# Performance work log

Hardware: AMD Instinct MI355X
Metric: run time of the kernel (lower is better)

The kernel has to match this reference:

```python
import jax, jax.numpy as jnp
import numpy as np

# --- dimensions (must match init_kwargs / input_specs) ---
N = 512      # memory_size
WORD = 64    # word_size
R = 4        # num_reads
NW = 1       # num_writes
C = 512      # controller_output_size
B = 16       # batch
T = 32       # seq_len
MODES = 3    # num_read_modes
IF = R*WORD + R + NW*WORD + NW + NW*WORD + NW*WORD + R + NW + NW + R*MODES  # 471
EPS = 1e-8


def _parse_interface(v):
    # v: [B, IF] -> dict of gates/keys, mirroring _parse_interface_vector
    i = 0
    def take(n):
        nonlocal i
        s = v[:, i:i+n]
        i += n
        return s
    read_keys = take(R*WORD).reshape(-1, R, WORD)
    read_strengths = jax.nn.softplus(take(R))
    write_keys = take(NW*WORD).reshape(-1, NW, WORD)
    write_strengths = jax.nn.softplus(take(NW))
    erase_vectors = jax.nn.sigmoid(take(NW*WORD)).reshape(-1, NW, WORD)
    write_vectors = take(NW*WORD).reshape(-1, NW, WORD)
    free_gates = jax.nn.sigmoid(take(R))
    allocation_gates = jax.nn.sigmoid(take(NW))
    write_gates = jax.nn.sigmoid(take(NW))
    read_modes = jax.nn.softmax(take(R*MODES).reshape(-1, R, MODES), axis=-1)
    return dict(read_keys=read_keys, read_strengths=read_strengths,
                write_keys=write_keys, write_strengths=write_strengths,
                erase_vectors=erase_vectors, write_vectors=write_vectors,
                free_gates=free_gates, allocation_gates=allocation_gates,
                write_gates=write_gates, read_modes=read_modes)


def _content_weights(keys, strengths, memory):
    # cosine content addressing: keys [B,H,WORD], memory [B,N,WORD] -> [B,H,N]
    kn = keys * jax.lax.rsqrt(jnp.sum(keys*keys, -1, keepdims=True) + EPS)
    mn = memory * jax.lax.rsqrt(jnp.sum(memory*memory, -1, keepdims=True) + EPS)
    sim = jnp.einsum('bhw,bnw->bhn', kn, mn)
    return jax.nn.softmax(sim * strengths[..., None], axis=-1)


def _allocation(usage):
    # usage [B,N] -> allocation weighting [B,N] (DNC usage-sorted free-list)
    idx = jnp.argsort(usage, axis=-1)                      # ascending usage
    sorted_u = jnp.take_along_axis(usage, idx, axis=-1)
    cp = jnp.cumprod(sorted_u, axis=-1)
    excl = jnp.concatenate([jnp.ones_like(cp[:, :1]), cp[:, :-1]], axis=-1)
    a_sorted = (1.0 - sorted_u) * excl
    inv = jnp.argsort(idx, axis=-1)                        # unsort
    return jnp.take_along_axis(a_sorted, inv, axis=-1)


def _forward(controller_output, W_if, b_if):
    eye = jnp.eye(N, dtype=controller_output.dtype)

    def step(carry, ctrl_t):
        memory, rw, ww, link, prec, usage = carry
        p = _parse_interface(ctrl_t @ W_if + b_if)
        # write weights: content + allocation, gated
        wcw = _content_weights(p['write_keys'], p['write_strengths'], memory)  # [B,NW,N]
        alloc = _allocation(usage)[:, None, :]
        ag = p['allocation_gates'][..., None]
        wg = p['write_gates'][..., None]
        new_ww = wg * (ag * alloc + (1.0 - ag) * wcw)                           # [B,NW,N]
        # usage update (write bump then free-gate retention)
        ww_agg = 1.0 - jnp.prod(1.0 - new_ww, axis=1)                           # [B,N]
        u = usage + ww_agg - usage * ww_agg
        psi = jnp.prod(1.0 - p['free_gates'][..., None] * rw, axis=1)           # [B,N]
        new_usage = u * psi
        # memory erase + write
        erase_term = jnp.prod(1.0 - new_ww[:, :, :, None] * p['erase_vectors'][:, :, None, :], axis=1)
        new_mem = memory * erase_term + jnp.einsum('bhn,bhw->bnw', new_ww, p['write_vectors'])
        # temporal linkage (write heads summed as in the source)
        wsum = jnp.sum(new_ww, axis=1)                                          # [B,N]
        new_link = (1.0 - wsum[:, :, None] - wsum[:, None, :]) * link \
                   + wsum[:, :, None] * prec[:, None, :]
        new_link = new_link * (1.0 - eye)
        new_prec = (1.0 - jnp.sum(wsum, axis=-1, keepdims=True)) * prec + wsum
        # read weights: backward / content / forward modes
        rcw = _content_weights(p['read_keys'], p['read_strengths'], new_mem)    # [B,R,N]
        fwd = jnp.einsum('bij,brj->bri', new_link, rw)
        bwd = jnp.einsum('bji,brj->bri', new_link, rw)
        m = p['read_modes']
        new_rw = m[..., 0:1] * bwd + m[..., 1:2] * rcw + m[..., 2:3] * fwd      # [B,R,N]
        read_words = jnp.einsum('brn,bnw->brw', new_rw, new_mem)                # [B,R,WORD]
        return (new_mem, new_rw, new_ww, new_link, new_prec, new_usage), read_words

    dt = controller_output.dtype
    init = (jnp.zeros((B, N, WORD), dt),
            jnp.full((B, R, N), 1.0 / N, dt),
            jnp.full((B, NW, N), 1.0 / N, dt),
            jnp.zeros((B, N, N), dt),
            jnp.zeros((B, N), dt),
            jnp.zeros((B, N), dt))
    _, rws = jax.lax.scan(step, init, jnp.swapaxes(controller_output, 0, 1))
    return jnp.swapaxes(rws, 0, 1)  # [B,T,R,WORD]


def setup_inputs() -> dict:
    key = jax.random.key(0)
    k1, k2 = jax.random.split(key)
    controller_output = jax.random.normal(k1, (B, T, C), dtype=jnp.float32)
    W_if = jax.random.normal(k2, (C, IF), dtype=jnp.float32) * 0.05  # keep gates unsaturated
    b_if = jnp.zeros((IF,), dtype=jnp.float32)
    return {"controller_output": controller_output, "W_if": W_if, "b_if": b_if}


def reference(controller_output, W_if, b_if):
    return _forward(controller_output, W_if, b_if)
```

## Files before the change

kernel.cpp:

```cpp
#include <hip/hip_runtime.h>

#define NCELLS 512
#define WORD_SZ 64
#define RHEADS 4
#define BATCH 16
#define TSTEPS 32
#define IFSZ 471
#define EPSC 1e-8f
#define NSTRIPE 16

__device__ __forceinline__ float wave_sum(float v) {
#pragma unroll
  for (int m = 32; m >= 1; m >>= 1) v += __shfl_xor(v, m, 64);
  return v;
}
__device__ __forceinline__ float wave_max(float v) {
#pragma unroll
  for (int m = 32; m >= 1; m >>= 1) v = fmaxf(v, __shfl_xor(v, m, 64));
  return v;
}
__device__ __forceinline__ float block_sum(float v, float* s_red, int tid) {
  float w = wave_sum(v);
  if ((tid & 63) == 0) s_red[tid >> 6] = w;
  __syncthreads();
  float tot = 0.f;
#pragma unroll
  for (int i = 0; i < 8; i++) tot += s_red[i];
  __syncthreads();
  return tot;
}
__device__ __forceinline__ float block_max(float v, float* s_red, int tid) {
  float w = wave_max(v);
  if ((tid & 63) == 0) s_red[tid >> 6] = w;
  __syncthreads();
  float tot = s_red[0];
#pragma unroll
  for (int i = 1; i < 8; i++) tot = fmaxf(tot, s_red[i]);
  __syncthreads();
  return tot;
}
__device__ __forceinline__ float softplus_f(float x) {
  return fmaxf(x, 0.f) + log1pf(expf(-fabsf(x)));
}
__device__ __forceinline__ float sigmoid_f(float x) {
  return 1.f / (1.f + expf(-x));
}

__global__ void init_kernel(float* link, float* mem, float* rw, float* usage,
                            float* prec, float* wcwb, float* ppb) {
  size_t i = (size_t)blockIdx.x * blockDim.x + threadIdx.x;
  size_t stride = (size_t)gridDim.x * blockDim.x;
  const size_t nlink = (size_t)BATCH * NCELLS * NCELLS;
  const size_t nmem = (size_t)BATCH * NCELLS * WORD_SZ;
  const size_t nrw = (size_t)BATCH * RHEADS * NCELLS;
  const size_t nu = (size_t)BATCH * NCELLS;
  for (size_t x = i; x < nlink; x += stride) link[x] = 0.f;
  for (size_t x = i; x < nmem; x += stride) mem[x] = 0.f;
  for (size_t x = i; x < nrw; x += stride) rw[x] = 1.f / NCELLS;
  for (size_t x = i; x < nu; x += stride) {
    usage[x] = 0.f; prec[x] = 0.f;
    wcwb[x] = 1.f / NCELLS;
    ppb[0 * nu + x] = ((x & (NCELLS - 1)) == 0) ? 1.f : 0.f;
    ppb[1 * nu + x] = 1.f;
    ppb[2 * nu + x] = 1.f;
    ppb[3 * nu + x] = 1.f;
  }
}

__global__ __launch_bounds__(512) void iface_kernel(
    const float* __restrict__ ctrl, const float* __restrict__ W,
    const float* __restrict__ bif, float* __restrict__ iface) {
  int bt = blockIdx.x;
  int tid = threadIdx.x;
  __shared__ float s_ctrl[512];
  __shared__ float s_v[IFSZ];
  s_ctrl[tid] = ctrl[(size_t)bt * 512 + tid];
  __syncthreads();
  if (tid < IFSZ) {
    float acc = bif[tid];
#pragma unroll 8
    for (int k = 0; k < 512; k++) acc = fmaf(s_ctrl[k], W[(size_t)k * IFSZ + tid], acc);
    s_v[tid] = acc;
  }
  __syncthreads();
  if (tid < IFSZ) {
    float v = s_v[tid];
    float o;
    if (tid < 256) o = v;
    else if (tid < 260) o = softplus_f(v);
    else if (tid < 324) o = v;
    else if (tid < 325) o = softplus_f(v);
    else if (tid < 389) o = sigmoid_f(v);
    else if (tid < 453) o = v;
    else if (tid < 459) o = sigmoid_f(v);
    else {
      int g = (tid - 459) / 3;
      int base = 459 + g * 3;
      float a = s_v[base], b = s_v[base + 1], c = s_v[base + 2];
      float mx = fmaxf(a, fmaxf(b, c));
      float ea = expf(a - mx), eb = expf(b - mx), ec = expf(c - mx);
      o = expf(v - mx) / (ea + eb + ec);
    }
    iface[(size_t)bt * IFSZ + tid] = o;
  }
}

__global__ __launch_bounds__(512) void step_link(
    const float* __restrict__ iface,
    const float* __restrict__ mem_old, float* __restrict__ mem_new,
    const float* __restrict__ usage_old, float* __restrict__ usage_new,
    const float* __restrict__ prec_old, float* __restrict__ prec_new,
    const float* __restrict__ rw_old,
    const float* __restrict__ wcwb, const float* __restrict__ ppb,
    float* __restrict__ link, float* __restrict__ fwd, float* __restrict__ bwdp,
    int t) {
  int stripe = blockIdx.x, b = blockIdx.y;
  int tid = threadIdx.x, lane = tid & 63, wid = tid >> 6;
  int n = tid;
  const float* ifc = iface + ((size_t)b * TSTEPS + t) * IFSZ;

  __shared__ float s_e[64], s_v[64];
  __shared__ float s_ww[512], s_prec[512], s_rw4[4][512];
  __shared__ float s_bpB[4][4][512];
  __shared__ float s_red[8];

  if (wid == 0 && stripe == 0) { s_e[lane] = ifc[325 + lane]; s_v[lane] = ifc[389 + lane]; }

  size_t bn = (size_t)b * NCELLS;
  const size_t BN = (size_t)BATCH * NCELLS;
  float u_n = usage_old[bn + n];
  float wcw = wcwb[bn + n];
  float p01 = ppb[0 * BN + bn + n] * ppb[1 * BN + bn + n];
  float p23 = ppb[2 * BN + bn + n] * ppb[3 * BN + bn + n];
  float allocv = (1.f - u_n) * (p01 * p23);
  float ag = ifc[457], wg = ifc[458];
  float wwn = wg * (ag * allocv + (1.f - ag) * wcw);
  s_ww[n] = wwn;
  s_prec[n] = prec_old[bn + n];
#pragma unroll
  for (int r = 0; r < 4; r++) s_rw4[r][n] = rw_old[(bn * RHEADS) + (size_t)r * NCELLS + n];
  __syncthreads();

  float* lbase = link + (size_t)b * NCELLS * NCELLS;
  int i0 = stripe * 32 + wid * 4;
  float wsi[4], rwi[4][4];
#pragma unroll
  for (int rr = 0; rr < 4; rr++) {
    wsi[rr] = s_ww[i0 + rr];
#pragma unroll
    for (int r = 0; r < 4; r++) rwi[rr][r] = s_rw4[r][i0 + rr];
  }
  float facc[4][4];
  float bc[4][8];
#pragma unroll
  for (int a = 0; a < 4; a++)
#pragma unroll
    for (int c = 0; c < 4; c++) facc[a][c] = 0.f;
#pragma unroll
  for (int a = 0; a < 4; a++)
#pragma unroll
    for (int c = 0; c < 8; c++) bc[a][c] = 0.f;

#pragma unroll
  for (int jj = 0; jj < 8; jj++) {
    int j = jj * 64 + lane;
    float swj = s_ww[j], spj = s_prec[j];
    float srw0 = s_rw4[0][j], srw1 = s_rw4[1][j], srw2 = s_rw4[2][j], srw3 = s_rw4[3][j];
#pragma unroll
    for (int rr = 0; rr < 4; rr++) {
      float* lp = lbase + (size_t)(i0 + rr) * NCELLS + j;
      float l = *lp;
      float ln = fmaf(1.f - wsi[rr] - swj, l, wsi[rr] * spj);
      if (j == i0 + rr) ln = 0.f;
      *lp = ln;
      facc[rr][0] = fmaf(ln, srw0, facc[rr][0]);
      facc[rr][1] = fmaf(ln, srw1, facc[rr][1]);
      facc[rr][2] = fmaf(ln, srw2, facc[rr][2]);
      facc[rr][3] = fmaf(ln, srw3, facc[rr][3]);
      bc[0][jj] = fmaf(ln, rwi[rr][0], bc[0][jj]);
      bc[1][jj] = fmaf(ln, rwi[rr][1], bc[1][jj]);
      bc[2][jj] = fmaf(ln, rwi[rr][2], bc[2][jj]);
      bc[3][jj] = fmaf(ln, rwi[rr][3], bc[3][jj]);
    }
  }
#pragma unroll
  for (int rr = 0; rr < 4; rr++) {
#pragma unroll
    for (int r = 0; r < 4; r++) facc[rr][r] = wave_sum(facc[rr][r]);
    if (lane == 0) {
#pragma unroll
      for (int r = 0; r < 4; r++)
        fwd[((size_t)b * RHEADS + r) * NCELLS + (i0 + rr)] = facc[rr][r];
    }
  }
  if (wid >= 4) {
#pragma unroll
    for (int r = 0; r < 4; r++)
#pragma unroll
      for (int jj = 0; jj < 8; jj++) s_bpB[wid - 4][r][jj * 64 + lane] = bc[r][jj];
  }
  __syncthreads();
  if (wid < 4) {
#pragma unroll
    for (int r = 0; r < 4; r++)
#pragma unroll
      for (int jj = 0; jj < 8; jj++) s_bpB[wid][r][jj * 64 + lane] += bc[r][jj];
  }
  __syncthreads();
#pragma unroll
  for (int r = 0; r < 4; r++) {
    float a = ((s_bpB[0][r][tid] + s_bpB[1][r][tid]) + (s_bpB[2][r][tid] + s_bpB[3][r][tid]));
    bwdp[(((size_t)stripe * BATCH + b) * RHEADS + r) * NCELLS + tid] = a;
  }

  if (stripe == 0) {
    const float* mo = mem_old + (size_t)b * NCELLS * WORD_SZ;
    float* mn = mem_new + (size_t)b * NCELLS * WORD_SZ;
#pragma unroll 4
    for (int kk = 0; kk < 64; kk++) {
      int flat = tid + kk * 512;
      int nn = flat >> 6, w = flat & 63;
      mn[flat] = fmaf(mo[flat], (1.f - s_ww[nn] * s_e[w]), s_ww[nn] * s_v[w]);
    }
  }
  if (stripe == 15) {
    float u = u_n + wwn - u_n * wwn;
    float psi = 1.f;
#pragma unroll
    for (int r = 0; r < 4; r++) psi *= (1.f - ifc[453 + r] * s_rw4[r][n]);
    usage_new[bn + n] = u * psi;
    float sw = block_sum(wwn, s_red, tid);
    prec_new[bn + n] = (1.f - sw) * s_prec[n] + wwn;
  }
}

__global__ __launch_bounds__(512) void read_step(
    const float* __restrict__ iface, const float* __restrict__ mem_new,
    const float* __restrict__ fwd, const float* __restrict__ bwdp,
    const float* __restrict__ usage_cur,
    float* __restrict__ rw_new, float* __restrict__ wcwb, float* __restrict__ ppb,
    float* __restrict__ out, int t) {
  int r = blockIdx.x, b = blockIdx.y;
  int tid = threadIdx.x, lane = tid & 63, wid = tid >> 6;
  int n = tid;
  const float* ifc = iface + ((size_t)b * TSTEPS + t) * IFSZ;
  bool have_next = (t + 1 < TSTEPS);
  const float* ifc2 = iface + ((size_t)b * TSTEPS + (have_next ? t + 1 : t)) * IFSZ;

  __shared__ float s_k[64], s_wk[64];
  __shared__ __align__(16) float s_u[512];
  __shared__ float s_rw[512];
  __shared__ float s_part[8][64];
  __shared__ float s_red[8];

  if (wid == 0) {
    float k = ifc[r * 64 + lane];
    float ss = wave_sum(k * k);
    s_k[lane] = k * rsqrtf(ss + EPSC);
  } else if (wid == 1 && have_next) {
    float k = ifc2[260 + lane];
    float ss = wave_sum(k * k);
    s_wk[lane] = k * rsqrtf(ss + EPSC);
  }
  if (have_next) s_u[tid] = usage_cur[(size_t)b * NCELLS + tid];
  __syncthreads();

  const float4* mrow = (const float4*)(mem_new + ((size_t)b * NCELLS + n) * WORD_SZ);
  bool do_w = (r == 0) && have_next;
  float msum = 0.f, dot = 0.f, dotw = 0.f;
#pragma unroll
  for (int i = 0; i < 16; i++) {
    float4 m4 = mrow[i];
    msum = fmaf(m4.x, m4.x, fmaf(m4.y, m4.y, fmaf(m4.z, m4.z, fmaf(m4.w, m4.w, msum))));
    dot = fmaf(m4.x, s_k[4 * i], fmaf(m4.y, s_k[4 * i + 1],
          fmaf(m4.z, s_k[4 * i + 2], fmaf(m4.w, s_k[4 * i + 3], dot))));
    if (do_w)
      dotw = fmaf(m4.x, s_wk[4 * i], fmaf(m4.y, s_wk[4 * i + 1],
             fmaf(m4.z, s_wk[4 * i + 2], fmaf(m4.w, s_wk[4 * i + 3], dotw))));
  }
  float minv = rsqrtf(msum + EPSC);
  float sim = dot * minv * ifc[256 + r];
  float mx = block_max(sim, s_red, tid);
  float e = expf(sim - mx);
  float ssum = block_sum(e, s_red, tid);
  float rcw = e / ssum;
  float bsum = 0.f;
#pragma unroll
  for (int s = 0; s < NSTRIPE; s++)
    bsum += bwdp[(((size_t)s * BATCH + b) * RHEADS + r) * NCELLS + n];
  float f = fwd[((size_t)b * RHEADS + r) * NCELLS + n];
  float m0 = ifc[459 + r * 3], m1 = ifc[459 + r * 3 + 1], m2 = ifc[459 + r * 3 + 2];
  float nrw = fmaf(m0, bsum, fmaf(m1, rcw, m2 * f));
  s_rw[n] = nrw;
  rw_new[((size_t)b * RHEADS + r) * NCELLS + n] = nrw;
  __syncthreads();

  float acc = 0.f;
  const float* mb = mem_new + (size_t)b * NCELLS * WORD_SZ;
#pragma unroll 8
  for (int k = 0; k < 64; k++) {
    int nn = wid * 64 + k;
    acc = fmaf(s_rw[nn], mb[(size_t)nn * WORD_SZ + lane], acc);
  }
  s_part[wid][lane] = acc;
  __syncthreads();
  if (tid < 64) {
    float a = 0.f;
#pragma unroll
    for (int w = 0; w < 8; w++) a += s_part[w][tid];
    out[(((size_t)b * TSTEPS + t) * RHEADS + r) * WORD_SZ + tid] = a;
  }

  if (have_next) {
    float un = s_u[n];
    int base = r * 128;
    float p0 = 1.f, p1 = 1.f, p2 = 1.f, p3 = 1.f;
#pragma unroll 8
    for (int j = 0; j < 128; j += 4) {
      float4 u4 = *(const float4*)&s_u[base + j];
      int ja = base + j;
      p0 *= (u4.x < un || (u4.x == un && (ja + 0) < n)) ? u4.x : 1.f;
      p1 *= (u4.y < un || (u4.y == un && (ja + 1) < n)) ? u4.y : 1.f;
      p2 *= (u4.z < un || (u4.z == un && (ja + 2) < n)) ? u4.z : 1.f;
      p3 *= (u4.w < un || (u4.w == un && (ja + 3) < n)) ? u4.w : 1.f;
    }
    ppb[((size_t)r * BATCH + b) * NCELLS + n] = (p0 * p1) * (p2 * p3);
    if (r == 0) {
      float simw = dotw * minv * ifc2[324];
      float mxw = block_max(simw, s_red, tid);
      float ew = expf(simw - mxw);
      float ssw = block_sum(ew, s_red, tid);
      wcwb[(size_t)b * NCELLS + n] = ew / ssw;
    }
  }
}

extern "C" void kernel_launch(void* const* d_in, const int* in_sizes, int n_in,
                              void* d_out, int out_size, void* d_ws, size_t ws_size,
                              hipStream_t stream) {
  const float* ctrl = (const float*)d_in[0];
  const float* Wif = (const float*)d_in[1];
  const float* bif = (const float*)d_in[2];
  float* out = (float*)d_out;

  float* p = (float*)d_ws;
  float* link = p;   p += (size_t)BATCH * NCELLS * NCELLS;
  float* mem0 = p;   p += (size_t)BATCH * NCELLS * WORD_SZ;
  float* mem1 = p;   p += (size_t)BATCH * NCELLS * WORD_SZ;
  float* iface = p;  p += (size_t)BATCH * TSTEPS * IFSZ;
  float* rw0 = p;    p += (size_t)BATCH * RHEADS * NCELLS;
  float* rw1 = p;    p += (size_t)BATCH * RHEADS * NCELLS;
  float* us0 = p;    p += (size_t)BATCH * NCELLS;
  float* us1 = p;    p += (size_t)BATCH * NCELLS;
  float* pr0 = p;    p += (size_t)BATCH * NCELLS;
  float* pr1 = p;    p += (size_t)BATCH * NCELLS;
  float* fwdb = p;   p += (size_t)BATCH * RHEADS * NCELLS;
  float* bwdp = p;   p += (size_t)NSTRIPE * BATCH * RHEADS * NCELLS;
  float* wcwb = p;   p += (size_t)BATCH * NCELLS;
  float* ppb = p;    p += (size_t)4 * BATCH * NCELLS;

  float* mem[2] = {mem0, mem1};
  float* rw[2] = {rw0, rw1};
  float* us[2] = {us0, us1};
  float* pr[2] = {pr0, pr1};

  hipLaunchKernelGGL(init_kernel, dim3(2048), dim3(256), 0, stream,
                     link, mem[0], rw[0], us[0], pr[0], wcwb, ppb);
  hipLaunchKernelGGL(iface_kernel, dim3(BATCH * TSTEPS), dim3(512), 0, stream,
                     ctrl, Wif, bif, iface);
  for (int t = 0; t < TSTEPS; t++) {
    int cu = t & 1;
    hipLaunchKernelGGL(step_link, dim3(NSTRIPE, BATCH), dim3(512), 0, stream,
                       iface, mem[cu], mem[cu ^ 1], us[cu], us[cu ^ 1],
                       pr[cu], pr[cu ^ 1], rw[cu], wcwb, ppb,
                       link, fwdb, bwdp, t);
    hipLaunchKernelGGL(read_step, dim3(RHEADS, BATCH), dim3(512), 0, stream,
                       iface, mem[cu ^ 1], fwdb, bwdp, us[cu ^ 1],
                       rw[cu ^ 1], wcwb, ppb, out, t);
  }
}
```

Before: 1.059 ms.

## Fuse timestep loop into persistent cooperative kernel with register-resident link matrix

Replaces the 64 per-timestep kernel launches with one cooperative persistent kernel of 256 blocks that loops over time and separates phases with grid-wide syncs. Each thread keeps its slice of the N×N link matrix in registers across all timesteps, so the 16 MB link matrix is no longer read and written in global memory each step, and its zero-initialisation is dropped. The memory update is now split across all stripes instead of one block. The costs are two grid syncs per step, high register pressure under launch_bounds(512,2), and a requirement that all 256 blocks be co-resident.

```diff
diff --git a/kernel.cpp b/kernel.cpp
--- a/kernel.cpp
+++ b/kernel.cpp
@@ -1,4 +1,7 @@
 #include <hip/hip_runtime.h>
+#include <hip/hip_cooperative_groups.h>
+
+namespace cg = cooperative_groups;
 
 #define NCELLS 512
 #define WORD_SZ 64
@@ -46,15 +49,13 @@
   return 1.f / (1.f + expf(-x));
 }
 
-__global__ void init_kernel(float* link, float* mem, float* rw, float* usage,
+__global__ void init_kernel(float* mem, float* rw, float* usage,
                             float* prec, float* wcwb, float* ppb) {
   size_t i = (size_t)blockIdx.x * blockDim.x + threadIdx.x;
   size_t stride = (size_t)gridDim.x * blockDim.x;
-  const size_t nlink = (size_t)BATCH * NCELLS * NCELLS;
   const size_t nmem = (size_t)BATCH * NCELLS * WORD_SZ;
   const size_t nrw = (size_t)BATCH * RHEADS * NCELLS;
   const size_t nu = (size_t)BATCH * NCELLS;
-  for (size_t x = i; x < nlink; x += stride) link[x] = 0.f;
   for (size_t x = i; x < nmem; x += stride) mem[x] = 0.f;
   for (size_t x = i; x < nrw; x += stride) rw[x] = 1.f / NCELLS;
   for (size_t x = i; x < nu; x += stride) {
@@ -105,233 +106,245 @@
   }
 }
 
-__global__ __launch_bounds__(512) void step_link(
+__global__ __launch_bounds__(512, 2) void dnc_loop(
     const float* __restrict__ iface,
-    const float* __restrict__ mem_old, float* __restrict__ mem_new,
-    const float* __restrict__ usage_old, float* __restrict__ usage_new,
-    const float* __restrict__ prec_old, float* __restrict__ prec_new,
-    const float* __restrict__ rw_old,
-    const float* __restrict__ wcwb, const float* __restrict__ ppb,
-    float* __restrict__ link, float* __restrict__ fwd, float* __restrict__ bwdp,
-    int t) {
-  int stripe = blockIdx.x, b = blockIdx.y;
-  int tid = threadIdx.x, lane = tid & 63, wid = tid >> 6;
-  int n = tid;
-  const float* ifc = iface + ((size_t)b * TSTEPS + t) * IFSZ;
-
+    float* __restrict__ mem0, float* __restrict__ mem1,
+    float* __restrict__ rw0, float* __restrict__ rw1,
+    float* __restrict__ us0, float* __restrict__ us1,
+    float* __restrict__ pr0, float* __restrict__ pr1,
+    float* __restrict__ wcwb, float* __restrict__ ppb,
+    float* __restrict__ fwdb, float* __restrict__ bwdp,
+    float* __restrict__ out) {
+  cg::grid_group grid = cg::this_grid();
+  const int blk = blockIdx.x;
+  const int stripe = blk >> 4, b = blk & 15;
+  const int tid = threadIdx.x, lane = tid & 63, wid = tid >> 6;
+  const int n = tid;
+  const size_t bn = (size_t)b * NCELLS;
+  const size_t BN = (size_t)BATCH * NCELLS;
+
+  __shared__ float s_ww[512], s_prec[512];
+  __shared__ float s_rw4[4][512];
+  __shared__ float s_bpB[4][4][512];
   __shared__ float s_e[64], s_v[64];
-  __shared__ float s_ww[512], s_prec[512], s_rw4[4][512];
-  __shared__ float s_bpB[4][4][512];
   __shared__ float s_red[8];
-
-  if (wid == 0 && stripe == 0) { s_e[lane] = ifc[325 + lane]; s_v[lane] = ifc[389 + lane]; }
-
-  size_t bn = (size_t)b * NCELLS;
-  const size_t BN = (size_t)BATCH * NCELLS;
-  float u_n = usage_old[bn + n];
-  float wcw = wcwb[bn + n];
-  float p01 = ppb[0 * BN + bn + n] * ppb[1 * BN + bn + n];
-  float p23 = ppb[2 * BN + bn + n] * ppb[3 * BN + bn + n];
-  float allocv = (1.f - u_n) * (p01 * p23);
-  float ag = ifc[457], wg = ifc[458];
-  float wwn = wg * (ag * allocv + (1.f - ag) * wcw);
-  s_ww[n] = wwn;
-  s_prec[n] = prec_old[bn + n];
-#pragma unroll
-  for (int r = 0; r < 4; r++) s_rw4[r][n] = rw_old[(bn * RHEADS) + (size_t)r * NCELLS + n];
-  __syncthreads();
-
-  float* lbase = link + (size_t)b * NCELLS * NCELLS;
-  int i0 = stripe * 32 + wid * 4;
-  float wsi[4], rwi[4][4];
-#pragma unroll
-  for (int rr = 0; rr < 4; rr++) {
-    wsi[rr] = s_ww[i0 + rr];
-#pragma unroll
-    for (int r = 0; r < 4; r++) rwi[rr][r] = s_rw4[r][i0 + rr];
-  }
-  float facc[4][4];
-  float bc[4][8];
-#pragma unroll
-  for (int a = 0; a < 4; a++)
-#pragma unroll
-    for (int c = 0; c < 4; c++) facc[a][c] = 0.f;
-#pragma unroll
-  for (int a = 0; a < 4; a++)
-#pragma unroll
-    for (int c = 0; c < 8; c++) bc[a][c] = 0.f;
-
-#pragma unroll
-  for (int jj = 0; jj < 8; jj++) {
-    int j = jj * 64 + lane;
-    float swj = s_ww[j], spj = s_prec[j];
-    float srw0 = s_rw4[0][j], srw1 = s_rw4[1][j], srw2 = s_rw4[2][j], srw3 = s_rw4[3][j];
-#pragma unroll
-    for (int rr = 0; rr < 4; rr++) {
-      float* lp = lbase + (size_t)(i0 + rr) * NCELLS + j;
-      float l = *lp;
-      float ln = fmaf(1.f - wsi[rr] - swj, l, wsi[rr] * spj);
-      if (j == i0 + rr) ln = 0.f;
-      *lp = ln;
-      facc[rr][0] = fmaf(ln, srw0, facc[rr][0]);
-      facc[rr][1] = fmaf(ln, srw1, facc[rr][1]);
-      facc[rr][2] = fmaf(ln, srw2, facc[rr][2]);
-      facc[rr][3] = fmaf(ln, srw3, facc[rr][3]);
-      bc[0][jj] = fmaf(ln, rwi[rr][0], bc[0][jj]);
-      bc[1][jj] = fmaf(ln, rwi[rr][1], bc[1][jj]);
-      bc[2][jj] = fmaf(ln, rwi[rr][2], bc[2][jj]);
-      bc[3][jj] = fmaf(ln, rwi[rr][3], bc[3][jj]);
-    }
-  }
-#pragma unroll
-  for (int rr = 0; rr < 4; rr++) {
-#pragma unroll
-    for (int r = 0; r < 4; r++) facc[rr][r] = wave_sum(facc[rr][r]);
-    if (lane == 0) {
-#pragma unroll
-      for (int r = 0; r < 4; r++)
-        fwd[((size_t)b * RHEADS + r) * NCELLS + (i0 + rr)] = facc[rr][r];
-    }
-  }
-  if (wid >= 4) {
-#pragma unroll
-    for (int r = 0; r < 4; r++)
-#pragma unroll
-      for (int jj = 0; jj < 8; jj++) s_bpB[wid - 4][r][jj * 64 + lane] = bc[r][jj];
-  }
-  __syncthreads();
-  if (wid < 4) {
-#pragma unroll
-    for (int r = 0; r < 4; r++)
-#pragma unroll
-      for (int jj = 0; jj < 8; jj++) s_bpB[wid][r][jj * 64 + lane] += bc[r][jj];
-  }
-  __syncthreads();
-#pragma unroll
-  for (int r = 0; r < 4; r++) {
-    float a = ((s_bpB[0][r][tid] + s_bpB[1][r][tid]) + (s_bpB[2][r][tid] + s_bpB[3][r][tid]));
-    bwdp[(((size_t)stripe * BATCH + b) * RHEADS + r) * NCELLS + tid] = a;
-  }
-
-  if (stripe == 0) {
-    const float* mo = mem_old + (size_t)b * NCELLS * WORD_SZ;
-    float* mn = mem_new + (size_t)b * NCELLS * WORD_SZ;
-#pragma unroll 4
-    for (int kk = 0; kk < 64; kk++) {
-      int flat = tid + kk * 512;
-      int nn = flat >> 6, w = flat & 63;
-      mn[flat] = fmaf(mo[flat], (1.f - s_ww[nn] * s_e[w]), s_ww[nn] * s_v[w]);
-    }
-  }
-  if (stripe == 15) {
-    float u = u_n + wwn - u_n * wwn;
-    float psi = 1.f;
-#pragma unroll
-    for (int r = 0; r < 4; r++) psi *= (1.f - ifc[453 + r] * s_rw4[r][n]);
-    usage_new[bn + n] = u * psi;
-    float sw = block_sum(wwn, s_red, tid);
-    prec_new[bn + n] = (1.f - sw) * s_prec[n] + wwn;
-  }
-}
-
-__global__ __launch_bounds__(512) void read_step(
-    const float* __restrict__ iface, const float* __restrict__ mem_new,
-    const float* __restrict__ fwd, const float* __restrict__ bwdp,
-    const float* __restrict__ usage_cur,
-    float* __restrict__ rw_new, float* __restrict__ wcwb, float* __restrict__ ppb,
-    float* __restrict__ out, int t) {
-  int r = blockIdx.x, b = blockIdx.y;
-  int tid = threadIdx.x, lane = tid & 63, wid = tid >> 6;
-  int n = tid;
-  const float* ifc = iface + ((size_t)b * TSTEPS + t) * IFSZ;
-  bool have_next = (t + 1 < TSTEPS);
-  const float* ifc2 = iface + ((size_t)b * TSTEPS + (have_next ? t + 1 : t)) * IFSZ;
-
   __shared__ float s_k[64], s_wk[64];
   __shared__ __align__(16) float s_u[512];
-  __shared__ float s_rw[512];
+  __shared__ float s_rwB[512];
   __shared__ float s_part[8][64];
-  __shared__ float s_red[8];
-
-  if (wid == 0) {
-    float k = ifc[r * 64 + lane];
-    float ss = wave_sum(k * k);
-    s_k[lane] = k * rsqrtf(ss + EPSC);
-  } else if (wid == 1 && have_next) {
-    float k = ifc2[260 + lane];
-    float ss = wave_sum(k * k);
-    s_wk[lane] = k * rsqrtf(ss + EPSC);
-  }
-  if (have_next) s_u[tid] = usage_cur[(size_t)b * NCELLS + tid];
-  __syncthreads();
-
-  const float4* mrow = (const float4*)(mem_new + ((size_t)b * NCELLS + n) * WORD_SZ);
-  bool do_w = (r == 0) && have_next;
-  float msum = 0.f, dot = 0.f, dotw = 0.f;
-#pragma unroll
-  for (int i = 0; i < 16; i++) {
-    float4 m4 = mrow[i];
-    msum = fmaf(m4.x, m4.x, fmaf(m4.y, m4.y, fmaf(m4.z, m4.z, fmaf(m4.w, m4.w, msum))));
-    dot = fmaf(m4.x, s_k[4 * i], fmaf(m4.y, s_k[4 * i + 1],
-          fmaf(m4.z, s_k[4 * i + 2], fmaf(m4.w, s_k[4 * i + 3], dot))));
-    if (do_w)
-      dotw = fmaf(m4.x, s_wk[4 * i], fmaf(m4.y, s_wk[4 * i + 1],
-             fmaf(m4.z, s_wk[4 * i + 2], fmaf(m4.w, s_wk[4 * i + 3], dotw))));
-  }
-  float minv = rsqrtf(msum + EPSC);
-  float sim = dot * minv * ifc[256 + r];
-  float mx = block_max(sim, s_red, tid);
-  float e = expf(sim - mx);
-  float ssum = block_sum(e, s_red, tid);
-  float rcw = e / ssum;
-  float bsum = 0.f;
-#pragma unroll
-  for (int s = 0; s < NSTRIPE; s++)
-    bsum += bwdp[(((size_t)s * BATCH + b) * RHEADS + r) * NCELLS + n];
-  float f = fwd[((size_t)b * RHEADS + r) * NCELLS + n];
-  float m0 = ifc[459 + r * 3], m1 = ifc[459 + r * 3 + 1], m2 = ifc[459 + r * 3 + 2];
-  float nrw = fmaf(m0, bsum, fmaf(m1, rcw, m2 * f));
-  s_rw[n] = nrw;
-  rw_new[((size_t)b * RHEADS + r) * NCELLS + n] = nrw;
-  __syncthreads();
-
-  float acc = 0.f;
-  const float* mb = mem_new + (size_t)b * NCELLS * WORD_SZ;
+
+  float lreg[4][8];
+#pragma unroll
+  for (int rr = 0; rr < 4; rr++)
+#pragma unroll
+    for (int jj = 0; jj < 8; jj++) lreg[rr][jj] = 0.f;
+
+  const int i0 = stripe * 32 + wid * 4;
+
+  for (int t = 0; t < TSTEPS; t++) {
+    const int cu = t & 1;
+    const float* mo = cu ? mem1 : mem0;  float* mn = cu ? mem0 : mem1;
+    const float* uo = cu ? us1 : us0;    float* unw = cu ? us0 : us1;
+    const float* po = cu ? pr1 : pr0;    float* pnw = cu ? pr0 : pr1;
+    const float* ro = cu ? rw1 : rw0;    float* rnw = cu ? rw0 : rw1;
+    const float* ifc = iface + ((size_t)b * TSTEPS + t) * IFSZ;
+
+    {
+      if (wid == 0) s_e[lane] = ifc[325 + lane];
+      else if (wid == 1) s_v[lane] = ifc[389 + lane];
+
+      float u_n = uo[bn + n];
+      float wcw = wcwb[bn + n];
+      float p01 = ppb[0 * BN + bn + n] * ppb[1 * BN + bn + n];
+      float p23 = ppb[2 * BN + bn + n] * ppb[3 * BN + bn + n];
+      float allocv = (1.f - u_n) * (p01 * p23);
+      float ag = ifc[457], wg = ifc[458];
+      float wwn = wg * (ag * allocv + (1.f - ag) * wcw);
+      s_ww[n] = wwn;
+      s_prec[n] = po[bn + n];
+#pragma unroll
+      for (int r = 0; r < 4; r++) s_rw4[r][n] = ro[bn * RHEADS + (size_t)r * NCELLS + n];
+      __syncthreads();
+
+      float wsi[4], rwi[4][4];
+#pragma unroll
+      for (int rr = 0; rr < 4; rr++) {
+        wsi[rr] = s_ww[i0 + rr];
+#pragma unroll
+        for (int r = 0; r < 4; r++) rwi[rr][r] = s_rw4[r][i0 + rr];
+      }
+      float facc[4][4];
+      float bc[4][8];
+#pragma unroll
+      for (int a = 0; a < 4; a++)
+#pragma unroll
+        for (int c = 0; c < 4; c++) facc[a][c] = 0.f;
+#pragma unroll
+      for (int a = 0; a < 4; a++)
+#pragma unroll
+        for (int c = 0; c < 8; c++) bc[a][c] = 0.f;
+
+#pragma unroll
+      for (int jj = 0; jj < 8; jj++) {
+        int j = jj * 64 + lane;
+        float swj = s_ww[j], spj = s_prec[j];
+        float srw0 = s_rw4[0][j], srw1 = s_rw4[1][j], srw2 = s_rw4[2][j], srw3 = s_rw4[3][j];
+#pragma unroll
+        for (int rr = 0; rr < 4; rr++) {
+          float ln = fmaf(1.f - wsi[rr] - swj, lreg[rr][jj], wsi[rr] * spj);
+          if (j == i0 + rr) ln = 0.f;
+          lreg[rr][jj] = ln;
+          facc[rr][0] = fmaf(ln, srw0, facc[rr][0]);
+          facc[rr][1] = fmaf(ln, srw1, facc[rr][1]);
+          facc[rr][2] = fmaf(ln, srw2, facc[rr][2]);
+          facc[rr][3] = fmaf(ln, srw3, facc[rr][3]);
+          bc[0][jj] = fmaf(ln, rwi[rr][0], bc[0][jj]);
+          bc[1][jj] = fmaf(ln, rwi[rr][1], bc[1][jj]);
+          bc[2][jj] = fmaf(ln, rwi[rr][2], bc[2][jj]);
+          bc[3][jj] = fmaf(ln, rwi[rr][3], bc[3][jj]);
+        }
+      }
+#pragma unroll
+      for (int rr = 0; rr < 4; rr++) {
+#pragma unroll
+        for (int r = 0; r < 4; r++) facc[rr][r] = wave_sum(facc[rr][r]);
+        if (lane == 0) {
+#pragma unroll
+          for (int r = 0; r < 4; r++)
+            fwdb[((size_t)b * RHEADS + r) * NCELLS + (i0 + rr)] = facc[rr][r];
+        }
+      }
+      if (wid >= 4) {
+#pragma unroll
+        for (int r = 0; r < 4; r++)
+#pragma unroll
+          for (int jj = 0; jj < 8; jj++) s_bpB[wid - 4][r][jj * 64 + lane] = bc[r][jj];
+      }
+      __syncthreads();
+      if (wid < 4) {
+#pragma unroll
+        for (int r = 0; r < 4; r++)
+#pragma unroll
+          for (int jj = 0; jj < 8; jj++) s_bpB[wid][r][jj * 64 + lane] += bc[r][jj];
+      }
+      __syncthreads();
+#pragma unroll
+      for (int r = 0; r < 4; r++) {
+        float a = (s_bpB[0][r][tid] + s_bpB[1][r][tid]) + (s_bpB[2][r][tid] + s_bpB[3][r][tid]);
+        bwdp[(((size_t)stripe * BATCH + b) * RHEADS + r) * NCELLS + tid] = a;
+      }
+
+      {
+        const float* mob = mo + (size_t)b * NCELLS * WORD_SZ + (size_t)stripe * 32 * WORD_SZ;
+        float* mnb = mn + (size_t)b * NCELLS * WORD_SZ + (size_t)stripe * 32 * WORD_SZ;
+#pragma unroll
+        for (int kk = 0; kk < 4; kk++) {
+          int flat = tid + kk * 512;
+          int nn = stripe * 32 + (flat >> 6), w = flat & 63;
+          mnb[flat] = fmaf(mob[flat], 1.f - s_ww[nn] * s_e[w], s_ww[nn] * s_v[w]);
+        }
+      }
+      if (stripe == 15) {
+        float u = u_n + wwn - u_n * wwn;
+        float psi = 1.f;
+#pragma unroll
+        for (int r = 0; r < 4; r++) psi *= (1.f - ifc[453 + r] * s_rw4[r][n]);
+        unw[bn + n] = u * psi;
+        float sw = block_sum(wwn, s_red, tid);
+        pnw[bn + n] = (1.f - sw) * s_prec[n] + wwn;
+      }
+    }
+    grid.sync();
+
+    if (blk < 64) {
+      const int r = blk & 3, b2 = blk >> 2;
+      const size_t b2n = (size_t)b2 * NCELLS;
+      const float* ifcB = iface + ((size_t)b2 * TSTEPS + t) * IFSZ;
+      bool have_next = (t + 1 < TSTEPS);
+      const float* ifc2 = iface + ((size_t)b2 * TSTEPS + (have_next ? t + 1 : t)) * IFSZ;
+
+      if (wid == 0) {
+        float k = ifcB[r * 64 + lane];
+        float ss = wave_sum(k * k);
+        s_k[lane] = k * rsqrtf(ss + EPSC);
+      } else if (wid == 1 && have_next) {
+        float k = ifc2[260 + lane];
+        float ss = wave_sum(k * k);
+        s_wk[lane] = k * rsqrtf(ss + EPSC);
+      }
+      if (have_next) s_u[tid] = unw[b2n + tid];
+      __syncthreads();
+
+      const float4* mrow = (const float4*)(mn + (b2n + n) * WORD_SZ);
+      bool do_w = (r == 0) && have_next;
+      float msum = 0.f, dot = 0.f, dotw = 0.f;
+#pragma unroll
+      for (int i = 0; i < 16; i++) {
+        float4 m4 = mrow[i];
+        msum = fmaf(m4.x, m4.x, fmaf(m4.y, m4.y, fmaf(m4.z, m4.z, fmaf(m4.w, m4.w, msum))));
+        dot = fmaf(m4.x, s_k[4 * i], fmaf(m4.y, s_k[4 * i + 1],
+              fmaf(m4.z, s_k[4 * i + 2], fmaf(m4.w, s_k[4 * i + 3], dot))));
+        if (do_w)
+          dotw = fmaf(m4.x, s_wk[4 * i], fmaf(m4.y, s_wk[4 * i + 1],
+                 fmaf(m4.z, s_wk[4 * i + 2], fmaf(m4.w, s_wk[4 * i + 3], dotw))));
+      }
+      float minv = rsqrtf(msum + EPSC);
+      float sim = dot * minv * ifcB[256 + r];
+      float mx = block_max(sim, s_red, tid);
+      float e = expf(sim - mx);
+      float ssum = block_sum(e, s_red, tid);
+      float rcw = e / ssum;
+      float bsum = 0.f;
+#pragma unroll
+      for (int s = 0; s < NSTRIPE; s++)
+        bsum += bwdp[(((size_t)s * BATCH + b2) * RHEADS + r) * NCELLS + n];
+      float f = fwdb[((size_t)b2 * RHEADS + r) * NCELLS + n];
+      float m0 = ifcB[459 + r * 3], m1 = ifcB[459 + r * 3 + 1], m2 = ifcB[459 + r * 3 + 2];
+      float nrw = fmaf(m0, bsum, fmaf(m1, rcw, m2 * f));
+      s_rwB[n] = nrw;
+      rnw[(b2n * RHEADS) + (size_t)r * NCELLS + n] = nrw;
+      __syncthreads();
+
+      float acc = 0.f;
+      const float* mb = mn + b2n * WORD_SZ;
 #pragma unroll 8
-  for (int k = 0; k < 64; k++) {
-    int nn = wid * 64 + k;
-    acc = fmaf(s_rw[nn], mb[(size_t)nn * WORD_SZ + lane], acc);
-  }
-  s_part[wid][lane] = acc;
-  __syncthreads();
-  if (tid < 64) {
-    float a = 0.f;
-#pragma unroll
-    for (int w = 0; w < 8; w++) a += s_part[w][tid];
-    out[(((size_t)b * TSTEPS + t) * RHEADS + r) * WORD_SZ + tid] = a;
-  }
-
-  if (have_next) {
-    float un = s_u[n];
-    int base = r * 128;
-    float p0 = 1.f, p1 = 1.f, p2 = 1.f, p3 = 1.f;
+      for (int k = 0; k < 64; k++) {
+        int nn = wid * 64 + k;
+        acc = fmaf(s_rwB[nn], mb[(size_t)nn * WORD_SZ + lane], acc);
+      }
+      s_part[wid][lane] = acc;
+      __syncthreads();
+      if (tid < 64) {
+        float a = 0.f;
+#pragma unroll
+        for (int w = 0; w < 8; w++) a += s_part[w][tid];
+        out[(((size_t)b2 * TSTEPS + t) * RHEADS + r) * WORD_SZ + tid] = a;
+      }
+
+      if (have_next) {
+        float un = s_u[n];
+        int base = r * 128;
+        float p0 = 1.f, p1 = 1.f, p2 = 1.f, p3 = 1.f;
 #pragma unroll 8
-    for (int j = 0; j < 128; j += 4) {
-      float4 u4 = *(const float4*)&s_u[base + j];
-      int ja = base + j;
-      p0 *= (u4.x < un || (u4.x == un && (ja + 0) < n)) ? u4.x : 1.f;
-      p1 *= (u4.y < un || (u4.y == un && (ja + 1) < n)) ? u4.y : 1.f;
-      p2 *= (u4.z < un || (u4.z == un && (ja + 2) < n)) ? u4.z : 1.f;
-      p3 *= (u4.w < un || (u4.w == un && (ja + 3) < n)) ? u4.w : 1.f;
+        for (int j = 0; j < 128; j += 4) {
+          float4 u4 = *(const float4*)&s_u[base + j];
+          int ja = base + j;
+          p0 *= (u4.x < un || (u4.x == un && (ja + 0) < n)) ? u4.x : 1.f;
+          p1 *= (u4.y < un || (u4.y == un && (ja + 1) < n)) ? u4.y : 1.f;
+          p2 *= (u4.z < un || (u4.z == un && (ja + 2) < n)) ? u4.z : 1.f;
+          p3 *= (u4.w < un || (u4.w == un && (ja + 3) < n)) ? u4.w : 1.f;
+        }
+        ppb[((size_t)r * BATCH + b2) * NCELLS + n] = (p0 * p1) * (p2 * p3);
+        if (r == 0) {
+          float simw = dotw * minv * ifc2[324];
+          float mxw = block_max(simw, s_red, tid);
+          float ew = expf(simw - mxw);
+          float ssw = block_sum(ew, s_red, tid);
+          wcwb[b2n + n] = ew / ssw;
+        }
+      }
     }
-    ppb[((size_t)r * BATCH + b) * NCELLS + n] = (p0 * p1) * (p2 * p3);
-    if (r == 0) {
-      float simw = dotw * minv * ifc2[324];
-      float mxw = block_max(simw, s_red, tid);
-      float ew = expf(simw - mxw);
-      float ssw = block_sum(ew, s_red, tid);
-      wcwb[(size_t)b * NCELLS + n] = ew / ssw;
-    }
+    grid.sync();
   }
 }
 
@@ -344,7 +357,6 @@
   float* out = (float*)d_out;
 
   float* p = (float*)d_ws;
-  float* link = p;   p += (size_t)BATCH * NCELLS * NCELLS;
   float* mem0 = p;   p += (size_t)BATCH * NCELLS * WORD_SZ;
   float* mem1 = p;   p += (size_t)BATCH * NCELLS * WORD_SZ;
   float* iface = p;  p += (size_t)BATCH * TSTEPS * IFSZ;
@@ -359,23 +371,14 @@
   float* wcwb = p;   p += (size_t)BATCH * NCELLS;
   float* ppb = p;    p += (size_t)4 * BATCH * NCELLS;
 
-  float* mem[2] = {mem0, mem1};
-  float* rw[2] = {rw0, rw1};
-  float* us[2] = {us0, us1};
-  float* pr[2] = {pr0, pr1};
-
-  hipLaunchKernelGGL(init_kernel, dim3(2048), dim3(256), 0, stream,
-                     link, mem[0], rw[0], us[0], pr[0], wcwb, ppb);
+  hipLaunchKernelGGL(init_kernel, dim3(256), dim3(256), 0, stream,
+                     mem0, rw0, us0, pr0, wcwb, ppb);
   hipLaunchKernelGGL(iface_kernel, dim3(BATCH * TSTEPS), dim3(512), 0, stream,
                      ctrl, Wif, bif, iface);
-  for (int t = 0; t < TSTEPS; t++) {
-    int cu = t & 1;
-    hipLaunchKernelGGL(step_link, dim3(NSTRIPE, BATCH), dim3(512), 0, stream,
-                       iface, mem[cu], mem[cu ^ 1], us[cu], us[cu ^ 1],
-                       pr[cu], pr[cu ^ 1], rw[cu], wcwb, ppb,
-                       link, fwdb, bwdp, t);
-    hipLaunchKernelGGL(read_step, dim3(RHEADS, BATCH), dim3(512), 0, stream,
-                       iface, mem[cu ^ 1], fwdb, bwdp, us[cu ^ 1],
-                       rw[cu ^ 1], wcwb, ppb, out, t);
-  }
-}
+
+  void* args[] = {(void*)&iface, (void*)&mem0, (void*)&mem1,
+                  (void*)&rw0, (void*)&rw1, (void*)&us0, (void*)&us1,
+                  (void*)&pr0, (void*)&pr1, (void*)&wcwb, (void*)&ppb,
+                  (void*)&fwdb, (void*)&bwdp, (void*)&out};
+  hipLaunchCooperativeKernel((void*)dnc_loop, dim3(256), dim3(512), args, 0, stream);
+}
```

Measured after the change: 2.730 ms. +157.9%, slower.
